# Kernel optimization log

Measured on AMD Instinct MI355X. Metric: run time of the kernel, lower is better.

The kernel has to match this reference:

```python
import jax, jax.numpy as jnp
import numpy as np

N, E = 20000, 200000
HID, NH, L = 128, 8, 7
DH = HID // NH
SCALE = float(np.sqrt(DH))
NNUM = 5
MLP_IN = HID + HID + 8 + 8 + 8 + NNUM  # 285
EPS = 1e-5


def _ln(x, g, b):
    mu = jnp.mean(x, -1, keepdims=True)
    var = jnp.mean((x - mu) ** 2, -1, keepdims=True)
    return (x - mu) * jax.lax.rsqrt(var + EPS) * g + b


def setup_inputs() -> dict:
    key = jax.random.key(0)
    ks = jax.random.split(key, 24)
    f = lambda k, s: (0.05 * jax.random.normal(k, s)).astype(jnp.float32)
    z = lambda s: jnp.zeros(s, jnp.float32)
    o = lambda s: jnp.ones(s, jnp.float32)
    inp = {
        'node_feats': f(ks[0], (N, 2)),
        'numericals': f(ks[1], (E, NNUM)),
        'W_emb': f(ks[2], (2, HID)), 'b_emb': z((HID,)),
        'WQ': f(ks[3], (L, HID, HID)), 'bQ': z((L, HID)),
        'WK': f(ks[4], (L, HID, HID)), 'bK': z((L, HID)),
        'WV': f(ks[5], (L, HID, HID)), 'bV': z((L, HID)),
        'WO': f(ks[6], (L, HID, HID)), 'bO': z((L, HID)),
        'ln1_g': o((L, HID)), 'ln1_b': z((L, HID)),
        'ln2_g': o((L, HID)), 'ln2_b': z((L, HID)),
        'W1': f(ks[7], (L, HID, HID)), 'b1': z((L, HID)),
        'W2': f(ks[8], (L, HID, HID)), 'b2': z((L, HID)),
        'curr_emb': f(ks[9], (15, 8)), 'pay_emb': f(ks[10], (7, 8)),
        'mlp_Wh': f(ks[11], (3, MLP_IN, MLP_IN)), 'mlp_bh': z((3, MLP_IN)),
        'mlp_Wo': f(ks[12], (MLP_IN, 2)), 'mlp_bo': z((2,)),
        'src': jax.random.randint(ks[13], (E,), 0, N, dtype=jnp.int32),
        'dst': jax.random.randint(ks[14], (E,), 0, N, dtype=jnp.int32),
        'payment_currency': jax.random.randint(ks[15], (E,), 0, 15, dtype=jnp.int32),
        'receiving_currency': jax.random.randint(ks[16], (E,), 0, 15, dtype=jnp.int32),
        'payment_format': jax.random.randint(ks[17], (E,), 0, 7, dtype=jnp.int32),
    }
    return inp


def reference(node_feats, numericals, W_emb, b_emb, WQ, bQ, WK, bK, WV, bV, WO, bO,
              ln1_g, ln1_b, ln2_g, ln2_b, W1, b1, W2, b2, curr_emb, pay_emb,
              mlp_Wh, mlp_bh, mlp_Wo, mlp_bo, src, dst,
              payment_currency, receiving_currency, payment_format):
    h = node_feats @ W_emb + b_emb  # [N, HID]
    for l in range(L):
        # --- graph multi-head attention (segment softmax over in-edges of dst) ---
        x = _ln(h, ln1_g[l], ln1_b[l])
        Q = (x @ WQ[l] + bQ[l]).reshape(N, NH, DH)
        K = (x @ WK[l] + bK[l]).reshape(N, NH, DH)
        V = (x @ WV[l] + bV[l]).reshape(N, NH, DH)
        scores = jnp.einsum('ehd,ehd->eh', Q[dst], K[src]) / SCALE  # [E, NH]
        m = jax.ops.segment_max(scores, dst, num_segments=N)        # [N, NH]
        ex = jnp.exp(scores - m[dst])
        den = jax.ops.segment_sum(ex, dst, num_segments=N)
        w = ex / den[dst]                                           # attn weights per edge
        attn = jax.ops.segment_sum(w[:, :, None] * V[src], dst, num_segments=N)
        h = h + attn.reshape(N, HID) @ WO[l] + bO[l]
        # --- FFN ---
        x = _ln(h, ln2_g[l], ln2_b[l])
        h = h + jax.nn.relu(x @ W1[l] + b1[l]) @ W2[l] + b2[l]
    # --- edge classifier ---
    ef = jnp.concatenate([curr_emb[payment_currency], curr_emb[receiving_currency],
                          pay_emb[payment_format], numericals], axis=1)  # [E, 29]
    y = jnp.concatenate([h[src], h[dst], ef], axis=1)  # [E, 285]
    for i in range(3):
        y = jax.nn.relu(y @ mlp_Wh[i] + mlp_bh[i])
    return y @ mlp_Wo + mlp_bo  # [E, 2]
```

## Files before the change

### kernel.cpp

```cpp
#include <hip/hip_runtime.h>

#define HID 128
#define NH 8
#define DH 16
#define NLAYERS 7
#define MLP_IN 285
#define MP 288
#define LDW 296
#define XS 136

typedef short short8 __attribute__((ext_vector_type(8)));
typedef float f32x4 __attribute__((ext_vector_type(4)));
typedef float f32x16 __attribute__((ext_vector_type(16)));
typedef unsigned short ushort8 __attribute__((ext_vector_type(8)));

__device__ inline unsigned short f2bf(float f) {
    union { float f; unsigned int u; } v; v.f = f;
    unsigned int r = v.u + 0x7FFF + ((v.u >> 16) & 1);
    return (unsigned short)(r >> 16);
}
__device__ inline float bf2f(unsigned short u) {
    union { unsigned int u; float f; } v; v.u = ((unsigned int)u) << 16;
    return v.f;
}

__global__ __launch_bounds__(256) void embed_kernel(
    const float* __restrict__ nf, const float* __restrict__ We,
    const float* __restrict__ be, float* __restrict__ h, int N)
{
    int idx = blockIdx.x * 256 + threadIdx.x;
    if (idx >= N * HID) return;
    int n = idx >> 7, j = idx & 127;
    h[idx] = fmaf(nf[n * 2], We[j], fmaf(nf[n * 2 + 1], We[HID + j], be[j]));
}

__global__ __launch_bounds__(256) void prep_nodew_kernel(
    const float* __restrict__ WQ, const float* __restrict__ WK,
    const float* __restrict__ WV, const float* __restrict__ WO,
    const float* __restrict__ W1, const float* __restrict__ W2,
    unsigned short* __restrict__ wnh, unsigned short* __restrict__ wnl)
{
    int idx = blockIdx.x * 256 + threadIdx.x;
    if (idx >= 42 * 32 * 64) return;
    int lane = idx & 63;
    int r = idx >> 6;
    int kt = r & 7; r >>= 3;
    int ct = r & 3; r >>= 2;
    int m = r;
    int l = m / 6, wi = m - l * 6;
    const float* Wb;
    switch (wi) {
        case 0: Wb = WQ; break; case 1: Wb = WK; break; case 2: Wb = WV; break;
        case 3: Wb = WO; break; case 4: Wb = W1; break; default: Wb = W2; break;
    }
    Wb += (size_t)l * HID * HID;
    int n = ct * 32 + (lane & 31);
    int kb = kt * 16 + (lane >> 5) * 8;
    ushort8 vh, vl;
#pragma unroll
    for (int j = 0; j < 8; ++j) {
        float w = Wb[(size_t)(kb + j) * HID + n];
        unsigned short hi = f2bf(w);
        vh[j] = hi;
        vl[j] = f2bf(w - bf2f(hi));
    }
    *(ushort8*)&wnh[(size_t)idx * 8] = vh;
    *(ushort8*)&wnl[(size_t)idx * 8] = vl;
}

#define LOADB(m, BH, BL) do { \
    size_t fb_ = (((size_t)(matbase + (m)) * 32 + (size_t)wave * 8) * 64 + lane) * 8; \
    const unsigned short* Bh_ = wnh + fb_; \
    const unsigned short* Bl_ = wnl + fb_; \
    _Pragma("unroll") \
    for (int kt = 0; kt < 8; ++kt) { \
        BH[kt] = *(const short8*)&Bh_[kt * 512]; \
        BL[kt] = *(const short8*)&Bl_[kt * 512]; \
    } \
} while (0)

#define COMPSTORE(BH, BL, BIAS, OUT, STRIDE, OFF) do { \
    f32x16 acc = {}; \
    _Pragma("unroll") \
    for (int kt = 0; kt < 8; ++kt) \
        acc = __builtin_amdgcn_mfma_f32_32x32x16_bf16(ah[kt], BH[kt], acc, 0, 0, 0); \
    _Pragma("unroll") \
    for (int kt = 0; kt < 8; ++kt) \
        acc = __builtin_amdgcn_mfma_f32_32x32x16_bf16(al[kt], BH[kt], acc, 0, 0, 0); \
    _Pragma("unroll") \
    for (int kt = 0; kt < 8; ++kt) \
        acc = __builtin_amdgcn_mfma_f32_32x32x16_bf16(ah[kt], BL[kt], acc, 0, 0, 0); \
    int col_ = wave * 32 + l31; \
    float bv_ = (BIAS)[col_]; \
    _Pragma("unroll") \
    for (int r = 0; r < 16; ++r) { \
        int rowm_ = (r & 3) + 8 * (r >> 2) + 4 * half; \
        int row_ = rowBase + rowm_; \
        if (row_ < M) (OUT)[(size_t)row_ * (STRIDE) + (OFF) + col_] = acc[r] + bv_; \
    } \
} while (0)

__global__ __launch_bounds__(256, 2) void ln_qkv_mfma(
    const float* __restrict__ h,
    const float* __restrict__ g, const float* __restrict__ bb,
    const unsigned short* __restrict__ wnh, const unsigned short* __restrict__ wnl,
    int matbase,
    const float* __restrict__ bQ, const float* __restrict__ bK, const float* __restrict__ bV,
    float* __restrict__ qo, float* __restrict__ kvo, int M)
{
    __shared__ unsigned short Xh[32][XS];
    __shared__ unsigned short Xl[32][XS];
    int tid = threadIdx.x;
    int lane = tid & 63, wave = tid >> 6;
    int rowBase = blockIdx.x * 32;

    for (int i = 0; i < 8; ++i) {
        int r = wave * 8 + i;
        int row = rowBase + r;
        float a0 = 0.f, a1 = 0.f;
        if (row < M) {
            a0 = h[(size_t)row * HID + lane];
            a1 = h[(size_t)row * HID + 64 + lane];
        }
        float s = a0 + a1;
#pragma unroll
        for (int off = 32; off > 0; off >>= 1) s += __shfl_down(s, off, 64);
        s = __shfl(s, 0, 64);
        float mu = s * (1.0f / 128.0f);
        float d0 = a0 - mu, d1 = a1 - mu;
        float v = d0 * d0 + d1 * d1;
#pragma unroll
        for (int off = 32; off > 0; off >>= 1) v += __shfl_down(v, off, 64);
        v = __shfl(v, 0, 64);
        float rr = rsqrtf(v * (1.0f / 128.0f) + 1e-5f);
        float x0 = d0 * rr * g[lane] + bb[lane];
        float x1 = d1 * rr * g[64 + lane] + bb[64 + lane];
        unsigned short h0 = f2bf(x0), h1 = f2bf(x1);
        Xh[r][lane] = h0;           Xh[r][64 + lane] = h1;
        Xl[r][lane] = f2bf(x0 - bf2f(h0));
        Xl[r][64 + lane] = f2bf(x1 - bf2f(h1));
    }
    __syncthreads();

    int l31 = lane & 31;
    int half = lane >> 5;

    short8 ah[8], al[8];
#pragma unroll
    for (int kt = 0; kt < 8; ++kt) {
        ah[kt] = *(const short8*)&Xh[l31][kt * 16 + half * 8];
        al[kt] = *(const short8*)&Xl[l31][kt * 16 + half * 8];
    }

    short8 bh0[8], bl0[8], bh1[8], bl1[8];
    LOADB(0, bh0, bl0);
    LOADB(1, bh1, bl1);
    COMPSTORE(bh0, bl0, bQ, qo, HID, 0);
    LOADB(2, bh0, bl0);
    COMPSTORE(bh1, bl1, bK, kvo, 256, 0);
    COMPSTORE(bh0, bl0, bV, kvo, 256, 128);
}

__global__ __launch_bounds__(256, 2) void post_mfma(
    const float* __restrict__ at, const float* __restrict__ hin,
    const unsigned short* __restrict__ wnh, const unsigned short* __restrict__ wnl,
    int matbase,
    const float* __restrict__ bO,
    const float* __restrict__ g2, const float* __restrict__ b2g,
    const float* __restrict__ b1, const float* __restrict__ b2,
    float* __restrict__ hout, int M)
{
    __shared__ unsigned short Ah[32][XS];
    __shared__ unsigned short Al[32][XS];
    __shared__ unsigned short Th[32][XS];
    __shared__ unsigned short Tl[32][XS];
    __shared__ float Hs[32][132];
    int tid = threadIdx.x;
    int lane = tid & 63, wave = tid >> 6;
    int rowBase = blockIdx.x * 32;
    int l31 = lane & 31;
    int half = lane >> 5;

    for (int i = tid; i < 32 * 32; i += 256) {
        int r = i >> 5, c4 = i & 31;
        int row = rowBase + r;
        float4 va = make_float4(0.f, 0.f, 0.f, 0.f), vh = va;
        if (row < M) {
            va = *(const float4*)&at[(size_t)row * HID + c4 * 4];
            vh = *(const float4*)&hin[(size_t)row * HID + c4 * 4];
        }
        const float* vp = (const float*)&va;
#pragma unroll
        for (int q = 0; q < 4; ++q) {
            unsigned short hi = f2bf(vp[q]);
            Ah[r][c4 * 4 + q] = hi;
            Al[r][c4 * 4 + q] = f2bf(vp[q] - bf2f(hi));
        }
        *(float4*)&Hs[r][c4 * 4] = vh;
    }
    __syncthreads();

    int colW = wave * 32 + l31;

    {
        short8 ah[8], al[8];
#pragma unroll
        for (int kt = 0; kt < 8; ++kt) {
            ah[kt] = *(const short8*)&Ah[l31][kt * 16 + half * 8];
            al[kt] = *(const short8*)&Al[l31][kt * 16 + half * 8];
        }
        short8 bh[8], bl[8];
        {
            size_t fb = (((size_t)(matbase + 3) * 32 + (size_t)wave * 8) * 64 + lane) * 8;
            const unsigned short* Bh = wnh + fb;
            const unsigned short* Bl = wnl + fb;
#pragma unroll
            for (int kt = 0; kt < 8; ++kt) {
                bh[kt] = *(const short8*)&Bh[kt * 512];
                bl[kt] = *(const short8*)&Bl[kt * 512];
            }
        }
        f32x16 acc = {};
#pragma unroll
        for (int kt = 0; kt < 8; ++kt)
            acc = __builtin_amdgcn_mfma_f32_32x32x16_bf16(ah[kt], bh[kt], acc, 0, 0, 0);
#pragma unroll
        for (int kt = 0; kt < 8; ++kt)
            acc = __builtin_amdgcn_mfma_f32_32x32x16_bf16(al[kt], bh[kt], acc, 0, 0, 0);
#pragma unroll
        for (int kt = 0; kt < 8; ++kt)
            acc = __builtin_amdgcn_mfma_f32_32x32x16_bf16(ah[kt], bl[kt], acc, 0, 0, 0);
        float bv = bO[colW];
#pragma unroll
        for (int r = 0; r < 16; ++r) {
            int rowm = (r & 3) + 8 * (r >> 2) + 4 * half;
            Hs[rowm][colW] += acc[r] + bv;
        }
    }
    __syncthreads();

    for (int i = 0; i < 8; ++i) {
        int r = wave * 8 + i;
        float a0 = Hs[r][lane];
        float a1 = Hs[r][64 + lane];
        float s = a0 + a1;
#pragma unroll
        for (int off = 32; off > 0; off >>= 1) s += __shfl_down(s, off, 64);
        s = __shfl(s, 0, 64);
        float mu = s * (1.0f / 128.0f);
        float d0 = a0 - mu, d1 = a1 - mu;
        float v = d0 * d0 + d1 * d1;
#pragma unroll
        for (int off = 32; off > 0; off >>= 1) v += __shfl_down(v, off, 64);
        v = __shfl(v, 0, 64);
        float rr = rsqrtf(v * (1.0f / 128.0f) + 1e-5f);
        float x0 = d0 * rr * g2[lane] + b2g[lane];
        float x1 = d1 * rr * g2[64 + lane] + b2g[64 + lane];
        unsigned short h0 = f2bf(x0), h1 = f2bf(x1);
        Ah[r][lane] = h0;           Ah[r][64 + lane] = h1;
        Al[r][lane] = f2bf(x0 - bf2f(h0));
        Al[r][64 + lane] = f2bf(x1 - bf2f(h1));
    }
    __syncthreads();

    {
        short8 ah[8], al[8];
#pragma unroll
        for (int kt = 0; kt < 8; ++kt) {
            ah[kt] = *(const short8*)&Ah[l31][kt * 16 + half * 8];
            al[kt] = *(const short8*)&Al[l31][kt * 16 + half * 8];
        }
        short8 bh[8], bl[8];
        {
            size_t fb = (((size_t)(matbase + 4) * 32 + (size_t)wave * 8) * 64 + lane) * 8;
            const unsigned short* Bh = wnh + fb;
            const unsigned short* Bl = wnl + fb;
#pragma unroll
            for (int kt = 0; kt < 8; ++kt) {
                bh[kt] = *(const short8*)&Bh[kt * 512];
                bl[kt] = *(const short8*)&Bl[kt * 512];
            }
        }
        f32x16 acc = {};
#pragma unroll
        for (int kt = 0; kt < 8; ++kt)
            acc = __builtin_amdgcn_mfma_f32_32x32x16_bf16(ah[kt], bh[kt], acc, 0, 0, 0);
#pragma unroll
        for (int kt = 0; kt < 8; ++kt)
            acc = __builtin_amdgcn_mfma_f32_32x32x16_bf16(al[kt], bh[kt], acc, 0, 0, 0);
#pragma unroll
        for (int kt = 0; kt < 8; ++kt)
            acc = __builtin_amdgcn_mfma_f32_32x32x16_bf16(ah[kt], bl[kt], acc, 0, 0, 0);
        float bv = b1[colW];
#pragma unroll
        for (int r = 0; r < 16; ++r) {
            int rowm = (r & 3) + 8 * (r >> 2) + 4 * half;
            float t = fmaxf(acc[r] + bv, 0.f);
            unsigned short hi = f2bf(t);
            Th[rowm][colW] = hi;
            Tl[rowm][colW] = f2bf(t - bf2f(hi));
        }
    }
    __syncthreads();

    {
        short8 ah[8], al[8];
#pragma unroll
        for (int kt = 0; kt < 8; ++kt) {
            ah[kt] = *(const short8*)&Th[l31][kt * 16 + half * 8];
            al[kt] = *(const short8*)&Tl[l31][kt * 16 + half * 8];
        }
        short8 bh[8], bl[8];
        {
            size_t fb = (((size_t)(matbase + 5) * 32 + (size_t)wave * 8) * 64 + lane) * 8;
            const unsigned short* Bh = wnh + fb;
            const unsigned short* Bl = wnl + fb;
#pragma unroll
            for (int kt = 0; kt < 8; ++kt) {
                bh[kt] = *(const short8*)&Bh[kt * 512];
                bl[kt] = *(const short8*)&Bl[kt * 512];
            }
        }
        f32x16 acc = {};
#pragma unroll
        for (int kt = 0; kt < 8; ++kt)
            acc = __builtin_amdgcn_mfma_f32_32x32x16_bf16(ah[kt], bh[kt], acc, 0, 0, 0);
#pragma unroll
        for (int kt = 0; kt < 8; ++kt)
            acc = __builtin_amdgcn_mfma_f32_32x32x16_bf16(al[kt], bh[kt], acc, 0, 0, 0);
#pragma unroll
        for (int kt = 0; kt < 8; ++kt)
            acc = __builtin_amdgcn_mfma_f32_32x32x16_bf16(ah[kt], bl[kt], acc, 0, 0, 0);
        float bv = b2[colW];
#pragma unroll
        for (int r = 0; r < 16; ++r) {
            int rowm = (r & 3) + 8 * (r >> 2) + 4 * half;
            int row = rowBase + rowm;
            if (row < M)
                hout[(size_t)row * HID + colW] = Hs[rowm][colW] + acc[r] + bv;
        }
    }
}

__global__ __launch_bounds__(256) void deg_kernel(
    const int* __restrict__ dst, int* __restrict__ deg, int E)
{
    int e = blockIdx.x * 256 + threadIdx.x;
    if (e < E) atomicAdd(&deg[dst[e]], 1);
}

__global__ __launch_bounds__(256) void scan_kernel(
    const int* __restrict__ deg, int* __restrict__ rowptr,
    int* __restrict__ cursor, int N)
{
    __shared__ int sums[256];
    int tid = threadIdx.x;
    int chunk = (N + 255) / 256;
    int lo = tid * chunk;
    int hi = lo + chunk; if (hi > N) hi = N;
    int s = 0;
    for (int i = lo; i < hi && i >= 0; ++i) s += deg[i];
    sums[tid] = s;
    __syncthreads();
    for (int off = 1; off < 256; off <<= 1) {
        int v = (tid >= off) ? sums[tid - off] : 0;
        __syncthreads();
        sums[tid] += v;
        __syncthreads();
    }
    int base = (tid == 0) ? 0 : sums[tid - 1];
    for (int i = lo; i < hi; ++i) {
        rowptr[i] = base; cursor[i] = base; base += deg[i];
    }
    if (tid == 255) rowptr[N] = sums[255];
}

__global__ __launch_bounds__(256) void scatter_kernel(
    const int* __restrict__ src, const int* __restrict__ dst,
    int* __restrict__ cursor, int* __restrict__ ssrc, int E)
{
    int e = blockIdx.x * 256 + threadIdx.x;
    if (e < E) {
        int p = atomicAdd(&cursor[dst[e]], 1);
        ssrc[p] = src[e];
    }
}

__global__ __launch_bounds__(256) void attn_fused_kernel(
    const float* __restrict__ q, const float* __restrict__ kv,
    const int* __restrict__ rowptr, const int* __restrict__ ssrc,
    float* __restrict__ at, int N)
{
    int node = blockIdx.x * 4 + (threadIdx.x >> 6);
    int lane = threadIdx.x & 63;
    if (node >= N) return;
    int beg = rowptr[node], end = rowptr[node + 1];
    float q0 = q[(size_t)node * HID + lane];
    float q1 = q[(size_t)node * HID + 64 + lane];
    float acc0 = 0.f, acc1 = 0.f, den0 = 0.f, den1 = 0.f;
    int i = beg;
    for (; i + 2 <= end; i += 2) {
        int s0 = ssrc[i], s1 = ssrc[i + 1];
        const float* kv0 = kv + (size_t)s0 * 256;
        const float* kv1 = kv + (size_t)s1 * 256;
        float k00 = kv0[lane],       k01 = kv0[64 + lane];
        float v00 = kv0[128 + lane], v01 = kv0[192 + lane];
        float k10 = kv1[lane],       k11 = kv1[64 + lane];
        float v10 = kv1[128 + lane], v11 = kv1[192 + lane];
        float p00 = q0 * k00, p01 = q1 * k01;
        float p10 = q0 * k10, p11 = q1 * k11;
#pragma unroll
        for (int off = 1; off < 16; off <<= 1) {
            p00 += __shfl_xor(p00, off, 64);
            p01 += __shfl_xor(p01, off, 64);
            p10 += __shfl_xor(p10, off, 64);
            p11 += __shfl_xor(p11, off, 64);
        }
        float w00 = __expf(p00 * 0.25f), w01 = __expf(p01 * 0.25f);
        float w10 = __expf(p10 * 0.25f), w11 = __expf(p11 * 0.25f);
        den0 += w00 + w10; den1 += w01 + w11;
        acc0 = fmaf(w10, v10, fmaf(w00, v00, acc0));
        acc1 = fmaf(w11, v11, fmaf(w01, v01, acc1));
    }
    if (i < end) {
        int s = ssrc[i];
        const float* kv0 = kv + (size_t)s * 256;
        float k0 = kv0[lane], k1 = kv0[64 + lane];
        float p0 = q0 * k0, p1 = q1 * k1;
#pragma unroll
        for (int off = 1; off < 16; off <<= 1) {
            p0 += __shfl_xor(p0, off, 64);
            p1 += __shfl_xor(p1, off, 64);
        }
        float w0 = __expf(p0 * 0.25f), w1 = __expf(p1 * 0.25f);
        den0 += w0; den1 += w1;
        acc0 = fmaf(w0, kv0[128 + lane], acc0);
        acc1 = fmaf(w1, kv0[192 + lane], acc1);
    }
    at[(size_t)node * HID + lane]      = (den0 > 0.f) ? acc0 / den0 : 0.f;
    at[(size_t)node * HID + 64 + lane] = (den1 > 0.f) ? acc1 / den1 : 0.f;
}

__global__ __launch_bounds__(256) void prep_wp_kernel(
    const float* __restrict__ Wh, unsigned short* __restrict__ wp)
{
    int idx = blockIdx.x * 256 + threadIdx.x;
    if (idx >= 3 * 9 * 18 * 64) return;
    int lane = idx & 63;
    int r = idx >> 6;
    int kt = r % 18; r /= 18;
    int ct = r % 9;
    int layer = r / 9;
    int n = ct * 32 + (lane & 31);
    int kbase = kt * 16 + (lane >> 5) * 8;
    ushort8 val;
#pragma unroll
    for (int j = 0; j < 8; ++j) {
        int k = kbase + j;
        float v = (n < MLP_IN && k < MLP_IN)
            ? Wh[(size_t)layer * MLP_IN * MLP_IN + (size_t)k * MLP_IN + n] : 0.f;
        val[j] = f2bf(v);
    }
    *(ushort8*)&wp[(size_t)idx * 8] = val;
}

__global__ __launch_bounds__(256) void prep_hb_kernel(
    const float* __restrict__ h, unsigned short* __restrict__ hb, int n)
{
    int idx = blockIdx.x * 256 + threadIdx.x;
    if (idx >= n) return;
    hb[idx] = f2bf(h[idx]);
}

#define ELOADB(ct, BUF) do { \
    const unsigned short* Wp_ = Wb + (size_t)(ct) * 9216; \
    _Pragma("unroll") \
    for (int kt = 0; kt < 18; ++kt) BUF[kt] = *(const short8*)&Wp_[kt * 512]; \
} while (0)

#define EMFMA(ct, BUF) do { \
    f32x16 acc = {}; \
    _Pragma("unroll") \
    for (int kt = 0; kt < 18; ++kt) \
        acc = __builtin_amdgcn_mfma_f32_32x32x16_bf16(afr[kt], BUF[kt], acc, 0, 0, 0); \
    int col_ = (ct) * 32 + l31; \
    if (col_ < MLP_IN) { \
        float bv_ = bias[col_]; \
        _Pragma("unroll") \
        for (int r = 0; r < 16; ++r) { \
            int rowm_ = (r & 3) + 8 * (r >> 2) + 4 * half; \
            y[(wave * 32 + rowm_) * LDW + col_] = f2bf(fmaxf(acc[r] + bv_, 0.f)); \
        } \
    } \
} while (0)

__global__ __launch_bounds__(256, 2) void edge_mlp_mfma(
    const unsigned short* __restrict__ hb, const float* __restrict__ ce,
    const float* __restrict__ pe, const float* __restrict__ num,
    const int* __restrict__ src, const int* __restrict__ dst,
    const int* __restrict__ pc, const int* __restrict__ rc,
    const int* __restrict__ pf,
    const unsigned short* __restrict__ wp, const float* __restrict__ bh,
    const float* __restrict__ Wo, const float* __restrict__ bo,
    float* __restrict__ out, int E)
{
    __shared__ unsigned short y[128 * LDW];
    int tid = threadIdx.x;
    int e0 = blockIdx.x * 128;

    for (int i = tid; i < 128 * 36; i += 256) {
        int t = i / 36;
        int c = i - t * 36;
        int e = e0 + t;
        if (e >= E) e = E - 1;
        ushort8 val;
        if (c < 16) {
            val = *(const ushort8*)&hb[(size_t)src[e] * HID + c * 8];
        } else if (c < 32) {
            val = *(const ushort8*)&hb[(size_t)dst[e] * HID + (c - 16) * 8];
        } else if (c == 32) {
            const float* p = &ce[pc[e] * 8];
#pragma unroll
            for (int j = 0; j < 8; ++j) val[j] = f2bf(p[j]);
        } else if (c == 33) {
            const float* p = &ce[rc[e] * 8];
#pragma unroll
            for (int j = 0; j < 8; ++j) val[j] = f2bf(p[j]);
        } else if (c == 34) {
            const float* p = &pe[pf[e] * 8];
#pragma unroll
            for (int j = 0; j < 8; ++j) val[j] = f2bf(p[j]);
        } else {
            const float* p = &num[(size_t)e * 5];
#pragma unroll
            for (int j = 0; j < 5; ++j) val[j] = f2bf(p[j]);
            val[5] = 0; val[6] = 0; val[7] = 0;
        }
        *(ushort8*)&y[t * LDW + c * 8] = val;
    }
    __syncthreads();

    int wave = tid >> 6;
    int lane = tid & 63;
    int l31 = lane & 31;
    int half = lane >> 5;
    int rowA = wave * 32 + l31;

    for (int layer = 0; layer < 3; ++layer) {
        const unsigned short* __restrict__ Wl = wp + (size_t)layer * 9 * 18 * 64 * 8;
        const float* __restrict__ bias = bh + layer * MLP_IN;
        const unsigned short* Wb = Wl + (size_t)lane * 8;

        short8 afr[18];
#pragma unroll
        for (int kt = 0; kt < 18; ++kt)
            afr[kt] = *(const short8*)&y[rowA * LDW + kt * 16 + half * 8];
        __syncthreads();

        short8 bA[18], bB[18];
        ELOADB(0, bA);
#pragma unroll
        for (int cp = 0; cp < 4; ++cp) {
            ELOADB(cp * 2 + 1, bB);
            EMFMA(cp * 2, bA);
            ELOADB(cp * 2 + 2, bA);
            EMFMA(cp * 2 + 1, bB);
        }
        EMFMA(8, bA);
        __syncthreads();
    }

    {
        int t = tid >> 1, oc = tid & 1;
        int e = e0 + t;
        if (e < E) {
            const unsigned short* yr = &y[t * LDW];
            float p0 = 0.f, p1 = 0.f, p2 = 0.f, p3 = 0.f;
            for (int kc = 0; kc < 35; ++kc) {
                ushort8 yv = *(const ushort8*)&yr[kc * 8];
                int kb = kc * 8;
                p0 = fmaf(bf2f(yv[0]), Wo[(kb + 0) * 2 + oc], p0);
                p1 = fmaf(bf2f(yv[1]), Wo[(kb + 1) * 2 + oc], p1);
                p2 = fmaf(bf2f(yv[2]), Wo[(kb + 2) * 2 + oc], p2);
                p3 = fmaf(bf2f(yv[3]), Wo[(kb + 3) * 2 + oc], p3);
                p0 = fmaf(bf2f(yv[4]), Wo[(kb + 4) * 2 + oc], p0);
                p1 = fmaf(bf2f(yv[5]), Wo[(kb + 5) * 2 + oc], p1);
                p2 = fmaf(bf2f(yv[6]), Wo[(kb + 6) * 2 + oc], p2);
                p3 = fmaf(bf2f(yv[7]), Wo[(kb + 7) * 2 + oc], p3);
            }
            float acc = bo[oc] + (p0 + p1) + (p2 + p3);
            for (int k = 280; k < MLP_IN; ++k)
                acc = fmaf(bf2f(yr[k]), Wo[k * 2 + oc], acc);
            out[(size_t)e * 2 + oc] = acc;
        }
    }
}

extern "C" void kernel_launch(void* const* d_in, const int* in_sizes, int n_in,
                              void* d_out, int out_size, void* d_ws, size_t ws_size,
                              hipStream_t stream)
{
    const float* node_feats = (const float*)d_in[0];
    const float* numericals = (const float*)d_in[1];
    const float* W_emb = (const float*)d_in[2];
    const float* b_emb = (const float*)d_in[3];
    const float* WQ = (const float*)d_in[4];
    const float* bQ = (const float*)d_in[5];
    const float* WK = (const float*)d_in[6];
    const float* bK = (const float*)d_in[7];
    const float* WV = (const float*)d_in[8];
    const float* bV = (const float*)d_in[9];
    const float* WO = (const float*)d_in[10];
    const float* bO = (const float*)d_in[11];
    const float* ln1_g = (const float*)d_in[12];
    const float* ln1_b = (const float*)d_in[13];
    const float* ln2_g = (const float*)d_in[14];
    const float* ln2_b = (const float*)d_in[15];
    const float* W1 = (const float*)d_in[16];
    const float* b1 = (const float*)d_in[17];
    const float* W2 = (const float*)d_in[18];
    const float* b2 = (const float*)d_in[19];
    const float* curr_emb = (const float*)d_in[20];
    const float* pay_emb = (const float*)d_in[21];
    const float* mlp_Wh = (const float*)d_in[22];
    const float* mlp_bh = (const float*)d_in[23];
    const float* mlp_Wo = (const float*)d_in[24];
    const float* mlp_bo = (const float*)d_in[25];
    const int* src = (const int*)d_in[26];
    const int* dst = (const int*)d_in[27];
    const int* pc = (const int*)d_in[28];
    const int* rc = (const int*)d_in[29];
    const int* pf = (const int*)d_in[30];

    const int N = in_sizes[0] / 2;
    const int E = in_sizes[26];

    float* ws = (float*)d_ws;
    float* h   = ws;
    float* qb  = h   + (size_t)N * HID;
    float* kvb = qb  + (size_t)N * HID;
    float* at  = kvb + (size_t)N * HID * 2;
    unsigned short* hb = (unsigned short*)(at + (size_t)N * HID);
    unsigned short* wpk = hb + (size_t)N * HID;
    unsigned short* wnh = wpk + (size_t)3 * 9 * 18 * 64 * 8;
    unsigned short* wnl = wnh + (size_t)42 * 32 * 64 * 8;
    int* rowptr = (int*)(wnl + (size_t)42 * 32 * 64 * 8);
    int* deg    = rowptr + (N + 1);
    int* cursor = deg + N;
    int* ssrc   = cursor + N;

    prep_wp_kernel<<<(3 * 9 * 18 * 64 + 255) / 256, 256, 0, stream>>>(mlp_Wh, wpk);
    prep_nodew_kernel<<<(42 * 32 * 64 + 255) / 256, 256, 0, stream>>>(
        WQ, WK, WV, WO, W1, W2, wnh, wnl);

    embed_kernel<<<(N * HID + 255) / 256, 256, 0, stream>>>(node_feats, W_emb, b_emb, h, N);

    hipMemsetAsync(deg, 0, (size_t)N * sizeof(int), stream);
    deg_kernel<<<(E + 255) / 256, 256, 0, stream>>>(dst, deg, E);
    scan_kernel<<<1, 256, 0, stream>>>(deg, rowptr, cursor, N);
    scatter_kernel<<<(E + 255) / 256, 256, 0, stream>>>(src, dst, cursor, ssrc, E);

    int nodeBlocks = (N + 31) / 32;

    for (int l = 0; l < NLAYERS; ++l) {
        ln_qkv_mfma<<<nodeBlocks, 256, 0, stream>>>(
            h, ln1_g + l * HID, ln1_b + l * HID,
            wnh, wnl, l * 6,
            bQ + l * HID, bK + l * HID, bV + l * HID,
            qb, kvb, N);

        attn_fused_kernel<<<(N + 3) / 4, 256, 0, stream>>>(qb, kvb, rowptr, ssrc, at, N);

        post_mfma<<<nodeBlocks, 256, 0, stream>>>(
            at, h, wnh, wnl, l * 6,
            bO + l * HID,
            ln2_g + l * HID, ln2_b + l * HID,
            b1 + l * HID, b2 + l * HID,
            h, N);
    }

    prep_hb_kernel<<<(N * HID + 255) / 256, 256, 0, stream>>>(h, hb, N * HID);

    edge_mlp_mfma<<<(E + 127) / 128, 256, 0, stream>>>(
        hb, curr_emb, pay_emb, numericals, src, dst, pc, rc, pf,
        wpk, mlp_bh, mlp_Wo, mlp_bo, (float*)d_out, E);
}
```

Baseline: 1.038 ms.

## Interleave K/V per lane for vectorized attention gather; half-tile MLP weight pipelining

The QKV kernel now writes K and V interleaved so each lane's two K and two V values sit together. The attention aggregation kernel can then fetch one float4 per lane per edge instead of four scalar loads, and it reduces each head over 8 lanes with 3 shuffles instead of 4. The edge MLP splits each column tile's weight fetch into two halves of 9 fragments, with sched_barrier, which lowers register pressure and keeps fine-grained load/compute overlap. The remaining GEMM code is macro cleanup, and the layout change couples the producer and consumer kernels.

```diff
diff --git a/kernel.cpp b/kernel.cpp
--- a/kernel.cpp
+++ b/kernel.cpp
@@ -79,7 +79,7 @@
     } \
 } while (0)
 
-#define COMPSTORE(BH, BL, BIAS, OUT, STRIDE, OFF) do { \
+#define COMPACC(BH, BL) \
     f32x16 acc = {}; \
     _Pragma("unroll") \
     for (int kt = 0; kt < 8; ++kt) \
@@ -89,16 +89,7 @@
         acc = __builtin_amdgcn_mfma_f32_32x32x16_bf16(al[kt], BH[kt], acc, 0, 0, 0); \
     _Pragma("unroll") \
     for (int kt = 0; kt < 8; ++kt) \
-        acc = __builtin_amdgcn_mfma_f32_32x32x16_bf16(ah[kt], BL[kt], acc, 0, 0, 0); \
-    int col_ = wave * 32 + l31; \
-    float bv_ = (BIAS)[col_]; \
-    _Pragma("unroll") \
-    for (int r = 0; r < 16; ++r) { \
-        int rowm_ = (r & 3) + 8 * (r >> 2) + 4 * half; \
-        int row_ = rowBase + rowm_; \
-        if (row_ < M) (OUT)[(size_t)row_ * (STRIDE) + (OFF) + col_] = acc[r] + bv_; \
-    } \
-} while (0)
+        acc = __builtin_amdgcn_mfma_f32_32x32x16_bf16(ah[kt], BL[kt], acc, 0, 0, 0);
 
 __global__ __launch_bounds__(256, 2) void ln_qkv_mfma(
     const float* __restrict__ h,
@@ -152,13 +143,43 @@
         al[kt] = *(const short8*)&Xl[l31][kt * 16 + half * 8];
     }
 
+    int col = wave * 32 + l31;
+    int kvpos = (col >> 1) * 4 + (col & 1);
+
     short8 bh0[8], bl0[8], bh1[8], bl1[8];
     LOADB(0, bh0, bl0);
     LOADB(1, bh1, bl1);
-    COMPSTORE(bh0, bl0, bQ, qo, HID, 0);
+    {
+        COMPACC(bh0, bl0);
+        float bv = bQ[col];
+#pragma unroll
+        for (int r = 0; r < 16; ++r) {
+            int rowm = (r & 3) + 8 * (r >> 2) + 4 * half;
+            int row = rowBase + rowm;
+            if (row < M) qo[(size_t)row * HID + col] = acc[r] + bv;
+        }
+    }
     LOADB(2, bh0, bl0);
-    COMPSTORE(bh1, bl1, bK, kvo, 256, 0);
-    COMPSTORE(bh0, bl0, bV, kvo, 256, 128);
+    {
+        COMPACC(bh1, bl1);
+        float bv = bK[col];
+#pragma unroll
+        for (int r = 0; r < 16; ++r) {
+            int rowm = (r & 3) + 8 * (r >> 2) + 4 * half;
+            int row = rowBase + rowm;
+            if (row < M) kvo[(size_t)row * 256 + kvpos] = acc[r] + bv;
+        }
+    }
+    {
+        COMPACC(bh0, bl0);
+        float bv = bV[col];
+#pragma unroll
+        for (int r = 0; r < 16; ++r) {
+            int rowm = (r & 3) + 8 * (r >> 2) + 4 * half;
+            int row = rowBase + rowm;
+            if (row < M) kvo[(size_t)row * 256 + kvpos + 2] = acc[r] + bv;
+        }
+    }
 }
 
 __global__ __launch_bounds__(256, 2) void post_mfma(
@@ -210,26 +231,8 @@
             al[kt] = *(const short8*)&Al[l31][kt * 16 + half * 8];
         }
         short8 bh[8], bl[8];
-        {
-            size_t fb = (((size_t)(matbase + 3) * 32 + (size_t)wave * 8) * 64 + lane) * 8;
-            const unsigned short* Bh = wnh + fb;
-            const unsigned short* Bl = wnl + fb;
-#pragma unroll
-            for (int kt = 0; kt < 8; ++kt) {
-                bh[kt] = *(const short8*)&Bh[kt * 512];
-                bl[kt] = *(const short8*)&Bl[kt * 512];
-            }
-        }
-        f32x16 acc = {};
-#pragma unroll
-        for (int kt = 0; kt < 8; ++kt)
-            acc = __builtin_amdgcn_mfma_f32_32x32x16_bf16(ah[kt], bh[kt], acc, 0, 0, 0);
-#pragma unroll
-        for (int kt = 0; kt < 8; ++kt)
-            acc = __builtin_amdgcn_mfma_f32_32x32x16_bf16(al[kt], bh[kt], acc, 0, 0, 0);
-#pragma unroll
-        for (int kt = 0; kt < 8; ++kt)
-            acc = __builtin_amdgcn_mfma_f32_32x32x16_bf16(ah[kt], bl[kt], acc, 0, 0, 0);
+        LOADB(3, bh, bl);
+        COMPACC(bh, bl);
         float bv = bO[colW];
 #pragma unroll
         for (int r = 0; r < 16; ++r) {
@@ -271,26 +274,8 @@
             al[kt] = *(const short8*)&Al[l31][kt * 16 + half * 8];
         }
         short8 bh[8], bl[8];
-        {
-            size_t fb = (((size_t)(matbase + 4) * 32 + (size_t)wave * 8) * 64 + lane) * 8;
-            const unsigned short* Bh = wnh + fb;
-            const unsigned short* Bl = wnl + fb;
-#pragma unroll
-            for (int kt = 0; kt < 8; ++kt) {
-                bh[kt] = *(const short8*)&Bh[kt * 512];
-                bl[kt] = *(const short8*)&Bl[kt * 512];
-            }
-        }
-        f32x16 acc = {};
-#pragma unroll
-        for (int kt = 0; kt < 8; ++kt)
-            acc = __builtin_amdgcn_mfma_f32_32x32x16_bf16(ah[kt], bh[kt], acc, 0, 0, 0);
-#pragma unroll
-        for (int kt = 0; kt < 8; ++kt)
-            acc = __builtin_amdgcn_mfma_f32_32x32x16_bf16(al[kt], bh[kt], acc, 0, 0, 0);
-#pragma unroll
-        for (int kt = 0; kt < 8; ++kt)
-            acc = __builtin_amdgcn_mfma_f32_32x32x16_bf16(ah[kt], bl[kt], acc, 0, 0, 0);
+        LOADB(4, bh, bl);
+        COMPACC(bh, bl);
         float bv = b1[colW];
 #pragma unroll
         for (int r = 0; r < 16; ++r) {
@@ -311,26 +296,8 @@
             al[kt] = *(const short8*)&Tl[l31][kt * 16 + half * 8];
         }
         short8 bh[8], bl[8];
-        {
-            size_t fb = (((size_t)(matbase + 5) * 32 + (size_t)wave * 8) * 64 + lane) * 8;
-            const unsigned short* Bh = wnh + fb;
-            const unsigned short* Bl = wnl + fb;
-#pragma unroll
-            for (int kt = 0; kt < 8; ++kt) {
-                bh[kt] = *(const short8*)&Bh[kt * 512];
-                bl[kt] = *(const short8*)&Bl[kt * 512];
-            }
-        }
-        f32x16 acc = {};
-#pragma unroll
-        for (int kt = 0; kt < 8; ++kt)
-            acc = __builtin_amdgcn_mfma_f32_32x32x16_bf16(ah[kt], bh[kt], acc, 0, 0, 0);
-#pragma unroll
-        for (int kt = 0; kt < 8; ++kt)
-            acc = __builtin_amdgcn_mfma_f32_32x32x16_bf16(al[kt], bh[kt], acc, 0, 0, 0);
-#pragma unroll
-        for (int kt = 0; kt < 8; ++kt)
-            acc = __builtin_amdgcn_mfma_f32_32x32x16_bf16(ah[kt], bl[kt], acc, 0, 0, 0);
+        LOADB(5, bh, bl);
+        COMPACC(bh, bl);
         float bv = b2[colW];
 #pragma unroll
         for (int r = 0; r < 16; ++r) {
@@ -395,50 +362,39 @@
     int lane = threadIdx.x & 63;
     if (node >= N) return;
     int beg = rowptr[node], end = rowptr[node + 1];
-    float q0 = q[(size_t)node * HID + lane];
-    float q1 = q[(size_t)node * HID + 64 + lane];
-    float acc0 = 0.f, acc1 = 0.f, den0 = 0.f, den1 = 0.f;
+    float2 q2 = *(const float2*)&q[(size_t)node * HID + lane * 2];
+    float ax = 0.f, ay = 0.f, den = 0.f;
     int i = beg;
     for (; i + 2 <= end; i += 2) {
         int s0 = ssrc[i], s1 = ssrc[i + 1];
-        const float* kv0 = kv + (size_t)s0 * 256;
-        const float* kv1 = kv + (size_t)s1 * 256;
-        float k00 = kv0[lane],       k01 = kv0[64 + lane];
-        float v00 = kv0[128 + lane], v01 = kv0[192 + lane];
-        float k10 = kv1[lane],       k11 = kv1[64 + lane];
-        float v10 = kv1[128 + lane], v11 = kv1[192 + lane];
-        float p00 = q0 * k00, p01 = q1 * k01;
-        float p10 = q0 * k10, p11 = q1 * k11;
-#pragma unroll
-        for (int off = 1; off < 16; off <<= 1) {
-            p00 += __shfl_xor(p00, off, 64);
-            p01 += __shfl_xor(p01, off, 64);
-            p10 += __shfl_xor(p10, off, 64);
-            p11 += __shfl_xor(p11, off, 64);
-        }
-        float w00 = __expf(p00 * 0.25f), w01 = __expf(p01 * 0.25f);
-        float w10 = __expf(p10 * 0.25f), w11 = __expf(p11 * 0.25f);
-        den0 += w00 + w10; den1 += w01 + w11;
-        acc0 = fmaf(w10, v10, fmaf(w00, v00, acc0));
-        acc1 = fmaf(w11, v11, fmaf(w01, v01, acc1));
+        float4 kv0 = *(const float4*)&kv[(size_t)s0 * 256 + lane * 4];
+        float4 kv1 = *(const float4*)&kv[(size_t)s1 * 256 + lane * 4];
+        float p0 = fmaf(q2.x, kv0.x, q2.y * kv0.y);
+        float p1 = fmaf(q2.x, kv1.x, q2.y * kv1.y);
+        p0 += __shfl_xor(p0, 1, 64); p1 += __shfl_xor(p1, 1, 64);
+        p0 += __shfl_xor(p0, 2, 64); p1 += __shfl_xor(p1, 2, 64);
+        p0 += __shfl_xor(p0, 4, 64); p1 += __shfl_xor(p1, 4, 64);
+        float w0 = __expf(p0 * 0.25f);
+        float w1 = __expf(p1 * 0.25f);
+        den += w0 + w1;
+        ax = fmaf(w1, kv1.z, fmaf(w0, kv0.z, ax));
+        ay = fmaf(w1, kv1.w, fmaf(w0, kv0.w, ay));
     }
     if (i < end) {
         int s = ssrc[i];
-        const float* kv0 = kv + (size_t)s * 256;
-        float k0 = kv0[lane], k1 = kv0[64 + lane];
-        float p0 = q0 * k0, p1 = q1 * k1;
-#pragma unroll
-        for (int off = 1; off < 16; off <<= 1) {
-            p0 += __shfl_xor(p0, off, 64);
-            p1 += __shfl_xor(p1, off, 64);
-        }
-        float w0 = __expf(p0 * 0.25f), w1 = __expf(p1 * 0.25f);
-        den0 += w0; den1 += w1;
-        acc0 = fmaf(w0, kv0[128 + lane], acc0);
-        acc1 = fmaf(w1, kv0[192 + lane], acc1);
-    }
-    at[(size_t)node * HID + lane]      = (den0 > 0.f) ? acc0 / den0 : 0.f;
-    at[(size_t)node * HID + 64 + lane] = (den1 > 0.f) ? acc1 / den1 : 0.f;
+        float4 kv0 = *(const float4*)&kv[(size_t)s * 256 + lane * 4];
+        float p0 = fmaf(q2.x, kv0.x, q2.y * kv0.y);
+        p0 += __shfl_xor(p0, 1, 64);
+        p0 += __shfl_xor(p0, 2, 64);
+        p0 += __shfl_xor(p0, 4, 64);
+        float w0 = __expf(p0 * 0.25f);
+        den += w0;
+        ax = fmaf(w0, kv0.z, ax);
+        ay = fmaf(w0, kv0.w, ay);
+    }
+    float inv = (den > 0.f) ? 1.f / den : 0.f;
+    float2 o; o.x = ax * inv; o.y = ay * inv;
+    *(float2*)&at[(size_t)node * HID + lane * 2] = o;
 }
 
 __global__ __launch_bounds__(256) void prep_wp_kernel(
@@ -472,26 +428,11 @@
     hb[idx] = f2bf(h[idx]);
 }
 
-#define ELOADB(ct, BUF) do { \
-    const unsigned short* Wp_ = Wb + (size_t)(ct) * 9216; \
+#define ELOADH(h, BUF) do { \
+    const unsigned short* Wp_ = Wb + (size_t)((h) >> 1) * 9216 + (size_t)((h) & 1) * 9 * 512; \
     _Pragma("unroll") \
-    for (int kt = 0; kt < 18; ++kt) BUF[kt] = *(const short8*)&Wp_[kt * 512]; \
-} while (0)
-
-#define EMFMA(ct, BUF) do { \
-    f32x16 acc = {}; \
-    _Pragma("unroll") \
-    for (int kt = 0; kt < 18; ++kt) \
-        acc = __builtin_amdgcn_mfma_f32_32x32x16_bf16(afr[kt], BUF[kt], acc, 0, 0, 0); \
-    int col_ = (ct) * 32 + l31; \
-    if (col_ < MLP_IN) { \
-        float bv_ = bias[col_]; \
-        _Pragma("unroll") \
-        for (int r = 0; r < 16; ++r) { \
-            int rowm_ = (r & 3) + 8 * (r >> 2) + 4 * half; \
-            y[(wave * 32 + rowm_) * LDW + col_] = f2bf(fmaxf(acc[r] + bv_, 0.f)); \
-        } \
-    } \
+    for (int j = 0; j < 9; ++j) BUF[j] = *(const short8*)&Wp_[j * 512]; \
+    __builtin_amdgcn_sched_barrier(0); \
 } while (0)
 
 __global__ __launch_bounds__(256, 2) void edge_mlp_mfma(
@@ -557,16 +498,29 @@
             afr[kt] = *(const short8*)&y[rowA * LDW + kt * 16 + half * 8];
         __syncthreads();
 
-        short8 bA[18], bB[18];
-        ELOADB(0, bA);
-#pragma unroll
-        for (int cp = 0; cp < 4; ++cp) {
-            ELOADB(cp * 2 + 1, bB);
-            EMFMA(cp * 2, bA);
-            ELOADB(cp * 2 + 2, bA);
-            EMFMA(cp * 2 + 1, bB);
-        }
-        EMFMA(8, bA);
+        short8 bA[9], bB[9];
+        ELOADH(0, bA);
+#pragma unroll
+        for (int ct = 0; ct < 9; ++ct) {
+            f32x16 acc = {};
+            ELOADH(2 * ct + 1, bB);
+#pragma unroll
+            for (int j = 0; j < 9; ++j)
+                acc = __builtin_amdgcn_mfma_f32_32x32x16_bf16(afr[j], bA[j], acc, 0, 0, 0);
+            if (ct < 8) ELOADH(2 * ct + 2, bA);
+#pragma unroll
+            for (int j = 0; j < 9; ++j)
+                acc = __builtin_amdgcn_mfma_f32_32x32x16_bf16(afr[9 + j], bB[j], acc, 0, 0, 0);
+            int col = ct * 32 + l31;
+            if (col < MLP_IN) {
+                float bv = bias[col];
+#pragma unroll
+                for (int r = 0; r < 16; ++r) {
+                    int rowm = (r & 3) + 8 * (r >> 2) + 4 * half;
+                    y[(wave * 32 + rowm) * LDW + col] = f2bf(fmaxf(acc[r] + bv, 0.f));
+                }
+            }
+        }
         __syncthreads();
     }
 
```

Measured after the change: 1.063 ms. 1.02x slower.
